# Kernel tuning notes

Measured on AMD Instinct MI355X. Metric: run time of the kernel, lower is better.

Reference implementation:

```python
import jax, jax.numpy as jnp
import numpy as np

SEQ_LEN = 2048
NUM_HEADS = 16
BATCH = 2
HEAD_DIM = 64


def setup_inputs() -> dict:
    key = jax.random.key(0)
    k_q, k_e1, k_e2 = jax.random.split(key, 3)
    q = jax.random.normal(k_q, (BATCH * NUM_HEADS, SEQ_LEN, HEAD_DIM), dtype=jnp.float32)
    e1 = jax.random.normal(k_e1, (SEQ_LEN, NUM_HEADS), dtype=jnp.float32)
    e2 = jax.random.normal(k_e2, (SEQ_LEN - 1, NUM_HEADS), dtype=jnp.float32)
    return {"q": q, "e1": e1, "e2": e2}


def reference(q, e1, e2):
    # The original double loop of overwriting scatters reduces to:
    #   ret[i, j] = e1[i - j]      if i >= j   (delta = i - j in [0, S-1])
    #   ret[i, j] = e2[j - i - 1]  if j > i    (j - i - 1 in [0, S-2])
    seq_len = e1.shape[0]
    num_heads = e1.shape[1]
    batch_x_heads = q.shape[0]
    batch_dim = batch_x_heads // num_heads

    i = jnp.arange(seq_len)[:, None]
    j = jnp.arange(seq_len)[None, :]
    delta = i - j  # (S, S)
    idx1 = jnp.clip(delta, 0, seq_len - 1)
    idx2 = jnp.clip(-delta - 1, 0, seq_len - 2)
    # (S, S, H): gather from e1 below/on diagonal, e2 above diagonal
    bias = jnp.where((delta >= 0)[:, :, None], e1[idx1], e2[idx2])
    bias = jnp.transpose(bias, (2, 0, 1))  # (H, S, S)
    ret = jnp.tile(bias, (batch_dim, 1, 1))  # (B*H, S, S)
    return ret
```

## Files before the change

kernel.cpp:

```cpp
#include <hip/hip_runtime.h>

#define S    2048
#define H    16
#define BH   32
#define ROWS 32
#define TPB  256
#define TILES_PER_H (S / ROWS)

typedef float f32x4 __attribute__((ext_vector_type(4)));

__global__ __launch_bounds__(TPB) void relpos_kernel(
    const float* __restrict__ e1,
    const float* __restrict__ e2,
    float* __restrict__ out)
{
    __shared__ float M[2 * S];

    const int tile = blockIdx.x & (TILES_PER_H - 1);
    const int h    = blockIdx.x >> 6;
    const int tid  = threadIdx.x;

    for (int u = tid; u < 2 * S - 1; u += TPB) {
        float v;
        if (u >= S - 1) v = e1[(u - (S - 1)) * H + h];
        else            v = e2[((S - 2) - u) * H + h];
        M[u] = v;
    }
    __syncthreads();

    const int ibase = tile * ROWS;
    float* out0 = out + (size_t)h * S * S;
    float* out1 = out + (size_t)(h + H) * S * S;

    for (int r = 0; r < ROWS; ++r) {
        const int i = ibase + r;
        const size_t rowoff = (size_t)i * S;
        #pragma unroll
        for (int k = 0; k < S / (TPB * 4); ++k) {
            const int j  = (tid + k * TPB) * 4;
            const int u0 = i - j + (S - 1);
            f32x4 v;
            v.x = M[u0];
            v.y = M[u0 - 1];
            v.z = M[u0 - 2];
            v.w = M[u0 - 3];
            __builtin_nontemporal_store(v, (f32x4*)(out0 + rowoff + j));
            __builtin_nontemporal_store(v, (f32x4*)(out1 + rowoff + j));
        }
    }
}

extern "C" void kernel_launch(void* const* d_in, const int* in_sizes, int n_in,
                              void* d_out, int out_size, void* d_ws, size_t ws_size,
                              hipStream_t stream) {
    const float* e1 = (const float*)d_in[1];
    const float* e2 = (const float*)d_in[2];
    float* out = (float*)d_out;

    const int grid = H * TILES_PER_H;
    relpos_kernel<<<grid, TPB, 0, stream>>>(e1, e2, out);
}
```

Measured before the change: 108.1 us.

## Reuse a register window of the bias table across rows and use plain stores

Reverses the shared-memory bias table so each thread loads a contiguous 36-element window with vector LDS loads once per column chunk. It then produces all 32 rows from registers by sliding the window. This removes repeated scalar LDS reads per store. Nontemporal stores are replaced by ordinary stores, which changes cache behaviour for the large streaming output. Register use goes up.

```diff
diff --git a/kernel.cpp b/kernel.cpp
--- a/kernel.cpp
+++ b/kernel.cpp
@@ -2,7 +2,6 @@
 
 #define S    2048
 #define H    16
-#define BH   32
 #define ROWS 32
 #define TPB  256
 #define TILES_PER_H (S / ROWS)
@@ -14,39 +13,44 @@
     const float* __restrict__ e2,
     float* __restrict__ out)
 {
-    __shared__ float M[2 * S];
+    __shared__ __align__(16) float R[2 * S];
 
     const int tile = blockIdx.x & (TILES_PER_H - 1);
     const int h    = blockIdx.x >> 6;
     const int tid  = threadIdx.x;
 
-    for (int u = tid; u < 2 * S - 1; u += TPB) {
-        float v;
-        if (u >= S - 1) v = e1[(u - (S - 1)) * H + h];
-        else            v = e2[((S - 2) - u) * H + h];
-        M[u] = v;
+    for (int v = tid; v < 2 * S - 1; v += TPB) {
+        float val;
+        if (v <= S - 1) val = e1[(S - 1 - v) * H + h];
+        else            val = e2[(v - S) * H + h];
+        R[v] = val;
     }
     __syncthreads();
 
     const int ibase = tile * ROWS;
-    float* out0 = out + (size_t)h * S * S;
-    float* out1 = out + (size_t)(h + H) * S * S;
+    float* const out0 = out + (size_t)h * S * S + (size_t)ibase * S;
+    float* const out1 = out0 + (size_t)H * S * S;
 
-    for (int r = 0; r < ROWS; ++r) {
-        const int i = ibase + r;
-        const size_t rowoff = (size_t)i * S;
+    #pragma unroll
+    for (int k = 0; k < 2; ++k) {
+        const int j0    = (tid + k * TPB) * 4;
+        const int wbase = (S - 1 - ibase) + j0 - 31;
+        f32x4 w4[9];
         #pragma unroll
-        for (int k = 0; k < S / (TPB * 4); ++k) {
-            const int j  = (tid + k * TPB) * 4;
-            const int u0 = i - j + (S - 1);
+        for (int c = 0; c < 9; ++c)
+            w4[c] = *(const f32x4*)&R[wbase + 4 * c];
+#define W(t) w4[(t) >> 2][(t) & 3]
+        #pragma unroll
+        for (int r = 0; r < ROWS; ++r) {
             f32x4 v;
-            v.x = M[u0];
-            v.y = M[u0 - 1];
-            v.z = M[u0 - 2];
-            v.w = M[u0 - 3];
-            __builtin_nontemporal_store(v, (f32x4*)(out0 + rowoff + j));
-            __builtin_nontemporal_store(v, (f32x4*)(out1 + rowoff + j));
+            v.x = W(31 - r);
+            v.y = W(32 - r);
+            v.z = W(33 - r);
+            v.w = W(34 - r);
+            *(f32x4*)(out0 + (size_t)r * S + j0) = v;
+            *(f32x4*)(out1 + (size_t)r * S + j0) = v;
         }
+#undef W
     }
 }
 
```

Result: no change. 107.4 us (-0.7%).
